# Kernel optimization log

Hardware: AMD Instinct MI355X
Metric: run time of the kernel (lower is better)

Reference implementation:

```python
import jax, jax.numpy as jnp
import numpy as np

EPS = 1e-12  # F.normalize default eps


def build_graph(src, tgt):
    # src,tgt: (b, wh, c). torch does this under no_grad -> stop_gradient.
    logits = jnp.einsum('bnc,bmc->bnm', src, tgt)      # (b, wh, wh)
    g = jax.nn.softmax(logits, axis=-1)                # row softmax
    g = g / jnp.clip(jnp.sum(jnp.abs(g), axis=-2, keepdims=True), EPS)  # L1 norm over dim=-2
    return jax.lax.stop_gradient(g)


def gconv(A, source, message, Wa, ba, Wu, bu):
    # Gconv (PCA-GM style): A @ relu(Linear_a(message)) + relu(Linear_u(source))
    ax = jax.nn.relu(jnp.einsum('bnc,cd->bnd', message, Wa) + ba)
    ux = jax.nn.relu(jnp.einsum('bnc,cd->bnd', source, Wu) + bu)
    return jnp.einsum('bnm,bmd->bnd', A, ax) + ux


def setup_inputs() -> dict:
    key = jax.random.key(0)
    ks = jax.random.split(key, 10)
    b, c, h, w = 4, 256, 64, 64
    scale = 1.0 / np.sqrt(c)
    inp = {
        'skt': jax.random.normal(ks[0], (b, c, h, w), jnp.float32),
        'ref': jax.random.normal(ks[1], (b, c, h, w), jnp.float32),
        'Wa3': jax.random.normal(ks[2], (c, c), jnp.float32) * scale,
        'ba3': jnp.zeros((c,), jnp.float32),
        'Wu3': jax.random.normal(ks[3], (c, c), jnp.float32) * scale,
        'bu3': jnp.zeros((c,), jnp.float32),
        'Wa4': jax.random.normal(ks[4], (c, c), jnp.float32) * scale,
        'ba4': jnp.zeros((c,), jnp.float32),
        'Wu4': jax.random.normal(ks[5], (c, c), jnp.float32) * scale,
        'bu4': jnp.zeros((c,), jnp.float32),
    }
    return inp


def reference(skt, ref, Wa3, ba3, Wu3, bu3, Wa4, ba4, Wu4, bu4):
    b, c, h, w = skt.shape
    skt_f = skt.reshape(b, c, h * w).transpose(0, 2, 1)  # (b, wh, c)
    ref_f = ref.reshape(b, c, h * w).transpose(0, 2, 1)
    sr = build_graph(skt_f, ref_f)                       # (b, wh, wh)
    gen = gconv(sr, skt_f, ref_f, Wa3, ba3, Wu3, bu3) + skt_f
    gg = build_graph(gen, gen)
    ggen = gconv(gg, gen, gen, Wa4, ba4, Wu4, bu4) + gen
    return ggen
```

## Files before the change

kernel.cpp:

```cpp
#include <hip/hip_runtime.h>
#include <cstdint>
#include <cstddef>

#define WH 4096
#define CD 256
typedef long long i64;

typedef __attribute__((ext_vector_type(8))) _Float16 f16x8;
typedef __attribute__((ext_vector_type(4))) float f32x4;

#define AS1 __attribute__((address_space(1)))
#define AS3 __attribute__((address_space(3)))

__device__ __forceinline__ unsigned short f2h(float f) {
    _Float16 h = (_Float16)f;
    return __builtin_bit_cast(unsigned short, h);
}
__device__ __forceinline__ float h2f(unsigned short u) {
    return (float)__builtin_bit_cast(_Float16, u);
}
__device__ __forceinline__ void ld16_lds(const void* g, void* l) {
    __builtin_amdgcn_global_load_lds((AS1 void*)g, (AS3 void*)l, 16, 0, 0);
}

struct TransArgs {
    const float* src[8];
    unsigned short* dhi[8];
    unsigned short* dlo[8];
};
__global__ __launch_bounds__(256) void k_transN(TransArgs ta, int RR, int CC) {
    __shared__ float t[32][33];
    const float* s = ta.src[blockIdx.z];
    unsigned short* dhi = ta.dhi[blockIdx.z];
    unsigned short* dlo = ta.dlo[blockIdx.z];
    const int c0 = blockIdx.x * 32, r0 = blockIdx.y * 32;
    const int tx = threadIdx.x, ty = threadIdx.y;
#pragma unroll
    for (int i = 0; i < 4; ++i)
        t[ty + i * 8][tx] = s[(i64)(r0 + ty + i * 8) * CC + c0 + tx];
    __syncthreads();
#pragma unroll
    for (int i = 0; i < 4; ++i) {
        const i64 idx = (i64)(c0 + ty + i * 8) * RR + r0 + tx;
        const float v = t[tx][ty + i * 8];
        const unsigned short hi = f2h(v);
        dhi[idx] = hi;
        dlo[idx] = f2h(v - h2f(hi));
    }
}

template <int MODE, int SPLIT3>
__global__ __launch_bounds__(256) void k_gemm(
    const unsigned short* __restrict__ A, const unsigned short* __restrict__ A2, int lda, i64 sA,
    const unsigned short* __restrict__ B, const unsigned short* __restrict__ B2, int ldb, i64 sB,
    float* __restrict__ Cf, unsigned short* __restrict__ Chi, unsigned short* __restrict__ Clo,
    int ldc, i64 sC, int K,
    const float* __restrict__ bias,
    const unsigned short* __restrict__ addh, const unsigned short* __restrict__ addl) {
    __shared__ __align__(16) short lA[SPLIT3 ? 8192 : 4096];
    __shared__ __align__(16) short lB[SPLIT3 ? 8192 : 4096];
    const int z = blockIdx.z;
    A += (i64)z * sA; B += (i64)z * sB;
    if constexpr (SPLIT3) { A2 += (i64)z * sA; B2 += (i64)z * sB; }

    const int tid = threadIdx.x;
    const int w = tid >> 6, l = tid & 63;
    const int wm = w >> 1, wn = w & 1;
    const int bm = blockIdx.y * 128, bn = blockIdx.x * 128;
    const int l15 = l & 15, lq = l >> 4;

    f32x4 acc[4][4] = {};

    for (int kt = 0; kt < K; kt += 32) {
        __syncthreads();
#pragma unroll
        for (int rr = 0; rr < 2; ++rr) {
            const int r = w + rr * 4;
            const int kb = r >> 1, mh = r & 1;
            const int row = mh * 64 + l;
            const i64 ao = (i64)(bm + row) * lda + kt + kb * 8;
            const i64 bo = (i64)(bn + row) * ldb + kt + kb * 8;
            ld16_lds(A + ao, (char*)lA + r * 1024);
            ld16_lds(B + bo, (char*)lB + r * 1024);
            if constexpr (SPLIT3) {
                ld16_lds(A2 + ao, (char*)lA + 8192 + r * 1024);
                ld16_lds(B2 + bo, (char*)lB + 8192 + r * 1024);
            }
        }
        __syncthreads();
        f16x8 ah[4], bh[4], al[4], bl[4];
#pragma unroll
        for (int i = 0; i < 4; ++i) {
            const int ia = (lq * 128 + wm * 64 + i * 16 + l15) * 8;
            const int ib = (lq * 128 + wn * 64 + i * 16 + l15) * 8;
            ah[i] = *(const f16x8*)(lA + ia);
            bh[i] = *(const f16x8*)(lB + ib);
            if constexpr (SPLIT3) {
                al[i] = *(const f16x8*)(lA + 4096 + ia);
                bl[i] = *(const f16x8*)(lB + 4096 + ib);
            }
        }
#pragma unroll
        for (int i = 0; i < 4; ++i)
#pragma unroll
            for (int j = 0; j < 4; ++j) {
                acc[i][j] = __builtin_amdgcn_mfma_f32_16x16x32_f16(ah[i], bh[j], acc[i][j], 0, 0, 0);
                if constexpr (SPLIT3) {
                    acc[i][j] = __builtin_amdgcn_mfma_f32_16x16x32_f16(ah[i], bl[j], acc[i][j], 0, 0, 0);
                    acc[i][j] = __builtin_amdgcn_mfma_f32_16x16x32_f16(al[i], bh[j], acc[i][j], 0, 0, 0);
                }
            }
    }

#pragma unroll
    for (int i = 0; i < 4; ++i)
#pragma unroll
        for (int j = 0; j < 4; ++j) {
            const int n = bn + wn * 64 + j * 16 + l15;
            const int m0 = bm + wm * 64 + i * 16 + lq * 4;
            const float bv = bias[n];
            if constexpr (MODE == 1) {
                unsigned short hv[4], lv[4];
#pragma unroll
                for (int r = 0; r < 4; ++r) {
                    const float v = fmaxf(acc[i][j][r] + bv, 0.f);
                    hv[r] = f2h(v);
                    lv[r] = f2h(v - h2f(hv[r]));
                }
                const i64 tb = (i64)z * sC + (i64)n * ldc + m0;
                *(ushort4*)(Chi + tb) = make_ushort4(hv[0], hv[1], hv[2], hv[3]);
                *(ushort4*)(Clo + tb) = make_ushort4(lv[0], lv[1], lv[2], lv[3]);
            } else {
#pragma unroll
                for (int r = 0; r < 4; ++r) {
                    const i64 idx = (i64)z * sC + (i64)(m0 + r) * ldc + n;
                    float v = fmaxf(acc[i][j][r] + bv, 0.f);
                    v += h2f(addh[idx]) + h2f(addl[idx]);
                    Cf[idx] = v;
                }
            }
        }
}

__global__ __launch_bounds__(256) void k_logits(
    const unsigned short* __restrict__ A, const unsigned short* __restrict__ A2,
    const unsigned short* __restrict__ B, const unsigned short* __restrict__ B2,
    unsigned short* __restrict__ G, float2* __restrict__ rowP) {
    __shared__ __align__(16) short lA[8192];
    __shared__ __align__(16) short lB[8192];
    const int tid = threadIdx.x;
    const int w = tid >> 6, l = tid & 63;
    const int wm = w >> 1, wn = w & 1;
    const int bm = blockIdx.y * 128, bn = blockIdx.x * 128;
    const int l15 = l & 15, lq = l >> 4;

    f32x4 acc[4][4] = {};

    for (int kt = 0; kt < CD; kt += 32) {
        __syncthreads();
#pragma unroll
        for (int rr = 0; rr < 2; ++rr) {
            const int r = w + rr * 4;
            const int kb = r >> 1, mh = r & 1;
            const int row = mh * 64 + l;
            const i64 ao = (i64)(bm + row) * CD + kt + kb * 8;
            const i64 bo = (i64)(bn + row) * CD + kt + kb * 8;
            ld16_lds(A + ao, (char*)lA + r * 1024);
            ld16_lds(B + bo, (char*)lB + r * 1024);
            ld16_lds(A2 + ao, (char*)lA + 8192 + r * 1024);
            ld16_lds(B2 + bo, (char*)lB + 8192 + r * 1024);
        }
        __syncthreads();
        f16x8 ah[4], bh[4], al[4], bl[4];
#pragma unroll
        for (int i = 0; i < 4; ++i) {
            const int ia = (lq * 128 + wm * 64 + i * 16 + l15) * 8;
            const int ib = (lq * 128 + wn * 64 + i * 16 + l15) * 8;
            ah[i] = *(const f16x8*)(lA + ia);
            bh[i] = *(const f16x8*)(lB + ib);
            al[i] = *(const f16x8*)(lA + 4096 + ia);
            bl[i] = *(const f16x8*)(lB + 4096 + ib);
        }
#pragma unroll
        for (int i = 0; i < 4; ++i)
#pragma unroll
            for (int j = 0; j < 4; ++j) {
                acc[i][j] = __builtin_amdgcn_mfma_f32_16x16x32_f16(ah[i], bh[j], acc[i][j], 0, 0, 0);
                acc[i][j] = __builtin_amdgcn_mfma_f32_16x16x32_f16(ah[i], bl[j], acc[i][j], 0, 0, 0);
                acc[i][j] = __builtin_amdgcn_mfma_f32_16x16x32_f16(al[i], bh[j], acc[i][j], 0, 0, 0);
            }
    }

#pragma unroll
    for (int i = 0; i < 4; ++i)
#pragma unroll
        for (int r = 0; r < 4; ++r) {
            const int grow = bm + wm * 64 + i * 16 + lq * 4 + r;
            float m = fmaxf(fmaxf(acc[i][0][r], acc[i][1][r]), fmaxf(acc[i][2][r], acc[i][3][r]));
            m = fmaxf(m, __shfl_xor(m, 1));
            m = fmaxf(m, __shfl_xor(m, 2));
            m = fmaxf(m, __shfl_xor(m, 4));
            m = fmaxf(m, __shfl_xor(m, 8));
            float s = 0.f;
#pragma unroll
            for (int j = 0; j < 4; ++j) {
                const float es = __expf((acc[i][j][r] - m) * 0.5f);
                s += es * es;
                G[(i64)grow * WH + bn + wn * 64 + j * 16 + l15] = f2h(es * 256.f);
            }
            s += __shfl_xor(s, 1); s += __shfl_xor(s, 2);
            s += __shfl_xor(s, 4); s += __shfl_xor(s, 8);
            if (l15 == 0)
                rowP[(i64)(blockIdx.x * 2 + wn) * WH + grow] = make_float2(m, s);
        }
}

__global__ __launch_bounds__(256) void k_colpart(const unsigned short* __restrict__ G,
                                                 const float2* __restrict__ rowP,
                                                 float* __restrict__ o,
                                                 float* __restrict__ part) {
    __shared__ float os[64];
    __shared__ float fl[4][64];
    const int t = threadIdx.x;
    const int r0 = blockIdx.y * 64;
    if (t < 64) {
        float M = -3.4e38f, S = 0.f;
        for (int x = 0; x < 64; ++x) {
            const float2 p = rowP[(i64)x * WH + r0 + t];
            const float nm = fmaxf(M, p.x);
            S = S * __expf(M - nm) + p.y * __expf(p.x - nm);
            M = nm;
        }
        const float ov = M + __logf(S);
        os[t] = ov;
        if (blockIdx.x == 0) o[r0 + t] = ov;
    }
    __syncthreads();
    {
        const int jt = t & 3, r = t >> 2;
        fl[jt][r] = __expf(rowP[(i64)(blockIdx.x * 4 + jt) * WH + r0 + r].x - os[r])
                  * (1.f / 65536.f);
    }
    __syncthreads();
    const int j = blockIdx.x * 256 + t;
    const int jt = t >> 6;
    float ps = 0.f;
#pragma unroll 4
    for (int r = 0; r < 64; ++r) {
        const float gv = h2f(G[(i64)(r0 + r) * WH + j]);
        ps += gv * gv * fl[jt][r];
    }
    part[(i64)blockIdx.y * WH + j] = ps;
}

template <int FULL>
__global__ __launch_bounds__(256) void k_attn(
    const unsigned short* __restrict__ G, const float* __restrict__ o,
    const float2* __restrict__ rowP, const float* __restrict__ part,
    const unsigned short* __restrict__ Bh, const unsigned short* __restrict__ Bl,
    float* __restrict__ Pw) {
    __shared__ __align__(16) short lL[4096];
    __shared__ __align__(16) short lBh[4096];
    __shared__ __align__(16) short lBl[FULL ? 4096 : 8];
    __shared__ float lS[512];
    const int tid = threadIdx.x;
    const int w = tid >> 6, l = tid & 63;
    const int wm = w >> 1, wn = w & 1;
    const int bm = blockIdx.y * 128, bn = blockIdx.x * 128;
    const int l15 = l & 15, lq = l >> 4;
    const i64 koff = (i64)blockIdx.z * 512;

    {
        float C0 = 0.f, C1 = 0.f;
#pragma unroll 4
        for (int p = 0; p < 64; ++p) {
            C0 += part[(i64)p * WH + koff + tid];
            C1 += part[(i64)p * WH + koff + 256 + tid];
        }
        lS[tid] = 1.f / fmaxf(C0, 1e-12f);
        lS[tid + 256] = 1.f / fmaxf(C1, 1e-12f);
    }
    float o4[4];
#pragma unroll
    for (int i = 0; i < 4; ++i) o4[i] = o[bm + wm * 64 + i * 16 + l15];

    float fi[4];
    f32x4 acc[4][4] = {};
    for (int kt = 0; kt < 512; kt += 32) {
        __syncthreads();
#pragma unroll
        for (int rr = 0; rr < 2; ++rr) {
            const int r = w + rr * 4;
            const int kb = r >> 1, mh = r & 1;
            ld16_lds(G + (i64)(bm + mh * 64 + l) * WH + koff + kt + kb * 8,
                     (char*)lL + r * 1024);
        }
#pragma unroll
        for (int rr = 0; rr < 2; ++rr) {
            const int r = w + rr * 4;
            const int kb = r >> 1, mh = r & 1;
            const i64 bo = (i64)(bn + mh * 64 + l) * WH + koff + kt + kb * 8;
            ld16_lds(Bh + bo, (char*)lBh + r * 1024);
            if constexpr (FULL) ld16_lds(Bl + bo, (char*)lBl + r * 1024);
        }
        if ((kt & 32) == 0) {
            const i64 half = (koff + kt) >> 6;
#pragma unroll
            for (int i = 0; i < 4; ++i)
                fi[i] = __expf(rowP[half * WH + bm + wm * 64 + i * 16 + l15].x - o4[i])
                      * (1.f / 65536.f);
        }
        __syncthreads();
        float sv[8];
        *(float4*)(sv)     = *(const float4*)(lS + kt + lq * 8);
        *(float4*)(sv + 4) = *(const float4*)(lS + kt + lq * 8 + 4);
        f16x8 bh[4], bl[4];
#pragma unroll
        for (int j = 0; j < 4; ++j) {
            const int ib = (lq * 128 + wn * 64 + j * 16 + l15) * 8;
            bh[j] = *(const f16x8*)(lBh + ib);
            if constexpr (FULL) bl[j] = *(const f16x8*)(lBl + ib);
        }
#pragma unroll
        for (int i = 0; i < 4; ++i) {
            const f16x8 graw = *(const f16x8*)(lL + (lq * 128 + wm * 64 + i * 16 + l15) * 8);
            const float fi_ = fi[i];
            f16x8 ah, al;
#pragma unroll
            for (int e = 0; e < 8; ++e) {
                const float gv = (float)graw[e];
                const float a = gv * gv * fi_ * sv[e];
                const _Float16 hh = (_Float16)a;
                ah[e] = hh;
                if constexpr (FULL) al[e] = (_Float16)(a - (float)hh);
            }
#pragma unroll
            for (int j = 0; j < 4; ++j) {
                acc[i][j] = __builtin_amdgcn_mfma_f32_16x16x32_f16(ah, bh[j], acc[i][j], 0, 0, 0);
                if constexpr (FULL) {
                    acc[i][j] = __builtin_amdgcn_mfma_f32_16x16x32_f16(ah, bl[j], acc[i][j], 0, 0, 0);
                    acc[i][j] = __builtin_amdgcn_mfma_f32_16x16x32_f16(al, bh[j], acc[i][j], 0, 0, 0);
                }
            }
        }
    }
    float* P = Pw + (i64)blockIdx.z * ((i64)WH * CD);
#pragma unroll
    for (int i = 0; i < 4; ++i)
#pragma unroll
        for (int j = 0; j < 4; ++j) {
            const int n = bn + wn * 64 + j * 16 + l15;
            const int m0 = bm + wm * 64 + i * 16 + lq * 4;
#pragma unroll
            for (int r = 0; r < 4; ++r)
                P[(i64)(m0 + r) * CD + n] = acc[i][j][r];
        }
}

template <int SPLIT>
__global__ __launch_bounds__(256) void k_red(const float* __restrict__ Pw,
                                             float* __restrict__ outp,
                                             unsigned short* __restrict__ hi,
                                             unsigned short* __restrict__ lo) {
    const i64 i = ((i64)blockIdx.x * 256 + threadIdx.x) * 4;
    float4 a = *(const float4*)(outp + i);
#pragma unroll
    for (int z = 0; z < 8; ++z) {
        const float4 p = *(const float4*)(Pw + (i64)z * ((i64)WH * CD) + i);
        a.x += p.x; a.y += p.y; a.z += p.z; a.w += p.w;
    }
    *(float4*)(outp + i) = a;
    if constexpr (SPLIT) {
        ushort4 h, l2;
        h.x = f2h(a.x); l2.x = f2h(a.x - h2f(h.x));
        h.y = f2h(a.y); l2.y = f2h(a.y - h2f(h.y));
        h.z = f2h(a.z); l2.z = f2h(a.z - h2f(h.z));
        h.w = f2h(a.w); l2.w = f2h(a.w - h2f(h.w));
        *(ushort4*)(hi + i) = h;
        *(ushort4*)(lo + i) = l2;
    }
}

extern "C" void kernel_launch(void* const* d_in, const int* in_sizes, int n_in,
                              void* d_out, int out_size, void* d_ws, size_t ws_size,
                              hipStream_t stream) {
    (void)in_sizes; (void)n_in; (void)out_size; (void)ws_size;
    const float* skt = (const float*)d_in[0];
    const float* ref = (const float*)d_in[1];
    const float* Wa3 = (const float*)d_in[2];
    const float* ba3 = (const float*)d_in[3];
    const float* Wu3 = (const float*)d_in[4];
    const float* bu3 = (const float*)d_in[5];
    const float* Wa4 = (const float*)d_in[6];
    const float* ba4 = (const float*)d_in[7];
    const float* Wu4 = (const float*)d_in[8];
    const float* bu4 = (const float*)d_in[9];
    float* out = (float*)d_out;

    const i64 WHC = (i64)WH * CD;
    const i64 GM  = (i64)WH * WH;
    const i64 CC  = (i64)CD * CD;

    auto al = [](size_t x) { return (x + 255) & ~(size_t)255; };
    char* p = (char*)d_ws; size_t off = 0;
    auto carve = [&](size_t bytes) { void* r = p + off; off += al(bytes); return r; };
    unsigned short* Gb    = (unsigned short*)carve((size_t)GM * 2);
    unsigned short* skthi = (unsigned short*)carve((size_t)4 * WHC * 2);
    unsigned short* sktlo = (unsigned short*)carve((size_t)4 * WHC * 2);
    unsigned short* refhi = (unsigned short*)carve((size_t)4 * WHC * 2);
    unsigned short* reflo = (unsigned short*)carve((size_t)4 * WHC * 2);
    unsigned short* ghi   = (unsigned short*)carve((size_t)4 * WHC * 2);
    unsigned short* glo   = (unsigned short*)carve((size_t)4 * WHC * 2);
    unsigned short* axthi = (unsigned short*)carve((size_t)4 * WHC * 2);
    unsigned short* axtlo = (unsigned short*)carve((size_t)4 * WHC * 2);
    float* ob             = (float*)carve((size_t)WH * 4);
    float* partb          = (float*)carve((size_t)64 * WH * 4);
    float2* rowPb         = (float2*)carve((size_t)64 * WH * 8);
    unsigned short* Wthi  = (unsigned short*)carve((size_t)4 * CC * 2);
    unsigned short* Wtlo  = (unsigned short*)carve((size_t)4 * CC * 2);
    float* Pw             = (float*)carve((size_t)8 * WHC * 4);

    dim3 thr(256), ttr(32, 8);
    {
        TransArgs ta{};
        for (int b = 0; b < 4; ++b) {
            ta.src[b] = skt + (i64)b * WHC;     ta.src[b + 4] = ref + (i64)b * WHC;
            ta.dhi[b] = skthi + (i64)b * WHC;   ta.dhi[b + 4] = refhi + (i64)b * WHC;
            ta.dlo[b] = sktlo + (i64)b * WHC;   ta.dlo[b + 4] = reflo + (i64)b * WHC;
        }
        k_transN<<<dim3(WH / 32, CD / 32, 8), ttr, 0, stream>>>(ta, CD, WH);
        TransArgs tw{};
        const float* ws[4] = { Wa3, Wu3, Wa4, Wu4 };
        for (int i = 0; i < 4; ++i) {
            tw.src[i] = ws[i];
            tw.dhi[i] = Wthi + (i64)i * CC;
            tw.dlo[i] = Wtlo + (i64)i * CC;
        }
        k_transN<<<dim3(CD / 32, CD / 32, 4), ttr, 0, stream>>>(tw, CD, CD);
    }

    auto stage = [&](const unsigned short* shi, const unsigned short* slo,
                     const unsigned short* mhi, const unsigned short* mlo,
                     int widx, const float* ba, const float* bu, float* outf,
                     unsigned short* ohi, unsigned short* olo, int FULL3) {
        if (FULL3)
            k_gemm<1, 1><<<dim3(CD / 128, WH / 128, 4), thr, 0, stream>>>(
                mhi, mlo, CD, WHC, Wthi + (i64)widx * CC, Wtlo + (i64)widx * CC, CD, 0,
                nullptr, axthi, axtlo, WH, WHC, CD, ba, nullptr, nullptr);
        else
            k_gemm<1, 0><<<dim3(CD / 128, WH / 128, 4), thr, 0, stream>>>(
                mhi, nullptr, CD, WHC, Wthi + (i64)widx * CC, nullptr, CD, 0,
                nullptr, axthi, axtlo, WH, WHC, CD, ba, nullptr, nullptr);
        if (FULL3)
            k_gemm<2, 1><<<dim3(CD / 128, WH / 128, 4), thr, 0, stream>>>(
                shi, slo, CD, WHC, Wthi + (i64)(widx + 1) * CC, Wtlo + (i64)(widx + 1) * CC, CD, 0,
                outf, nullptr, nullptr, CD, WHC, CD, bu, shi, slo);
        else
            k_gemm<2, 0><<<dim3(CD / 128, WH / 128, 4), thr, 0, stream>>>(
                shi, nullptr, CD, WHC, Wthi + (i64)(widx + 1) * CC, nullptr, CD, 0,
                outf, nullptr, nullptr, CD, WHC, CD, bu, shi, slo);
        for (int b = 0; b < 4; ++b) {
            k_logits<<<dim3(WH / 128, WH / 128, 1), thr, 0, stream>>>(
                shi + (i64)b * WHC, slo + (i64)b * WHC,
                mhi + (i64)b * WHC, mlo + (i64)b * WHC, Gb, rowPb);
            k_colpart<<<dim3(WH / 256, WH / 64, 1), thr, 0, stream>>>(Gb, rowPb, ob, partb);
            if (FULL3)
                k_attn<1><<<dim3(CD / 128, WH / 128, 8), thr, 0, stream>>>(
                    Gb, ob, rowPb, partb, axthi + (i64)b * WHC, axtlo + (i64)b * WHC, Pw);
            else
                k_attn<0><<<dim3(CD / 128, WH / 128, 8), thr, 0, stream>>>(
                    Gb, ob, rowPb, partb, axthi + (i64)b * WHC, nullptr, Pw);
            if (ohi)
                k_red<1><<<dim3((unsigned)(WHC / 1024)), thr, 0, stream>>>(
                    Pw, outf + (i64)b * WHC, ohi + (i64)b * WHC, olo + (i64)b * WHC);
            else
                k_red<0><<<dim3((unsigned)(WHC / 1024)), thr, 0, stream>>>(
                    Pw, outf + (i64)b * WHC, nullptr, nullptr);
        }
    };

    stage(skthi, sktlo, refhi, reflo, 0, ba3, bu3, out, ghi, glo, 1);
    stage(ghi, glo, ghi, glo, 2, ba4, bu4, out, nullptr, nullptr, 0);
}
```

Baseline: 1.118 ms.

## Enlarge logits tile to 256 rows and store attention partials in fp16

The logits kernel now computes a 256x128 tile per block with 8x4 accumulators per wave. This reuses each B fragment across twice as many A rows and halves the grid, at the cost of more registers and LDS. Separately, the split-K attention partials are written as fp16 instead of fp32, and the reduction converts them back. That halves partial-buffer traffic but drops precision in the partial sums, which may hurt accuracy.

```diff
diff --git a/kernel.cpp b/kernel.cpp
--- a/kernel.cpp
+++ b/kernel.cpp
@@ -142,60 +142,66 @@
         }
 }
 
-__global__ __launch_bounds__(256) void k_logits(
+__global__ __launch_bounds__(256, 2) void k_logits(
     const unsigned short* __restrict__ A, const unsigned short* __restrict__ A2,
     const unsigned short* __restrict__ B, const unsigned short* __restrict__ B2,
     unsigned short* __restrict__ G, float2* __restrict__ rowP) {
-    __shared__ __align__(16) short lA[8192];
+    __shared__ __align__(16) short lA[16384];
     __shared__ __align__(16) short lB[8192];
     const int tid = threadIdx.x;
     const int w = tid >> 6, l = tid & 63;
     const int wm = w >> 1, wn = w & 1;
-    const int bm = blockIdx.y * 128, bn = blockIdx.x * 128;
+    const int bm = blockIdx.y * 256, bn = blockIdx.x * 128;
     const int l15 = l & 15, lq = l >> 4;
 
-    f32x4 acc[4][4] = {};
+    f32x4 acc[8][4] = {};
 
     for (int kt = 0; kt < CD; kt += 32) {
         __syncthreads();
 #pragma unroll
-        for (int rr = 0; rr < 2; ++rr) {
+        for (int rr = 0; rr < 12; ++rr) {
             const int r = w + rr * 4;
-            const int kb = r >> 1, mh = r & 1;
-            const int row = mh * 64 + l;
-            const i64 ao = (i64)(bm + row) * CD + kt + kb * 8;
-            const i64 bo = (i64)(bn + row) * CD + kt + kb * 8;
-            ld16_lds(A + ao, (char*)lA + r * 1024);
-            ld16_lds(B + bo, (char*)lB + r * 1024);
-            ld16_lds(A2 + ao, (char*)lA + 8192 + r * 1024);
-            ld16_lds(B2 + bo, (char*)lB + 8192 + r * 1024);
-        }
-        __syncthreads();
-        f16x8 ah[4], bh[4], al[4], bl[4];
-#pragma unroll
-        for (int i = 0; i < 4; ++i) {
-            const int ia = (lq * 128 + wm * 64 + i * 16 + l15) * 8;
-            const int ib = (lq * 128 + wn * 64 + i * 16 + l15) * 8;
-            ah[i] = *(const f16x8*)(lA + ia);
-            bh[i] = *(const f16x8*)(lB + ib);
-            al[i] = *(const f16x8*)(lA + 4096 + ia);
-            bl[i] = *(const f16x8*)(lB + 4096 + ib);
-        }
-#pragma unroll
-        for (int i = 0; i < 4; ++i)
+            if (r < 32) {
+                const int ra = r & 15;
+                const int kb = ra >> 2, nh = ra & 3;
+                const i64 ao = (i64)(bm + nh * 64 + l) * CD + kt + kb * 8;
+                if (r < 16) ld16_lds(A + ao, (char*)lA + ra * 1024);
+                else        ld16_lds(A2 + ao, (char*)lA + 16384 + ra * 1024);
+            } else {
+                const int rb = r & 7;
+                const int kb = rb >> 1, mh = rb & 1;
+                const i64 bo = (i64)(bn + mh * 64 + l) * CD + kt + kb * 8;
+                if (r < 40) ld16_lds(B + bo, (char*)lB + rb * 1024);
+                else        ld16_lds(B2 + bo, (char*)lB + 8192 + rb * 1024);
+            }
+        }
+        __syncthreads();
+        f16x8 bh[4], bl[4];
+#pragma unroll
+        for (int j = 0; j < 4; ++j) {
+            const int ib = (lq * 128 + wn * 64 + j * 16 + l15) * 8;
+            bh[j] = *(const f16x8*)(lB + ib);
+            bl[j] = *(const f16x8*)(lB + 4096 + ib);
+        }
+#pragma unroll
+        for (int i = 0; i < 8; ++i) {
+            const int ia = (lq * 256 + wm * 128 + i * 16 + l15) * 8;
+            const f16x8 ah = *(const f16x8*)(lA + ia);
+            const f16x8 al = *(const f16x8*)(lA + 8192 + ia);
 #pragma unroll
             for (int j = 0; j < 4; ++j) {
-                acc[i][j] = __builtin_amdgcn_mfma_f32_16x16x32_f16(ah[i], bh[j], acc[i][j], 0, 0, 0);
-                acc[i][j] = __builtin_amdgcn_mfma_f32_16x16x32_f16(ah[i], bl[j], acc[i][j], 0, 0, 0);
-                acc[i][j] = __builtin_amdgcn_mfma_f32_16x16x32_f16(al[i], bh[j], acc[i][j], 0, 0, 0);
-            }
-    }
-
-#pragma unroll
-    for (int i = 0; i < 4; ++i)
+                acc[i][j] = __builtin_amdgcn_mfma_f32_16x16x32_f16(ah, bh[j], acc[i][j], 0, 0, 0);
+                acc[i][j] = __builtin_amdgcn_mfma_f32_16x16x32_f16(ah, bl[j], acc[i][j], 0, 0, 0);
+                acc[i][j] = __builtin_amdgcn_mfma_f32_16x16x32_f16(al, bh[j], acc[i][j], 0, 0, 0);
+            }
+        }
+    }
+
+#pragma unroll
+    for (int i = 0; i < 8; ++i)
 #pragma unroll
         for (int r = 0; r < 4; ++r) {
-            const int grow = bm + wm * 64 + i * 16 + lq * 4 + r;
+            const int grow = bm + wm * 128 + i * 16 + lq * 4 + r;
             float m = fmaxf(fmaxf(acc[i][0][r], acc[i][1][r]), fmaxf(acc[i][2][r], acc[i][3][r]));
             m = fmaxf(m, __shfl_xor(m, 1));
             m = fmaxf(m, __shfl_xor(m, 2));
@@ -258,7 +264,7 @@
     const unsigned short* __restrict__ G, const float* __restrict__ o,
     const float2* __restrict__ rowP, const float* __restrict__ part,
     const unsigned short* __restrict__ Bh, const unsigned short* __restrict__ Bl,
-    float* __restrict__ Pw) {
+    unsigned short* __restrict__ Pw) {
     __shared__ __align__(16) short lL[4096];
     __shared__ __align__(16) short lBh[4096];
     __shared__ __align__(16) short lBl[FULL ? 4096 : 8];
@@ -344,7 +350,7 @@
             }
         }
     }
-    float* P = Pw + (i64)blockIdx.z * ((i64)WH * CD);
+    unsigned short* P = Pw + (i64)blockIdx.z * ((i64)WH * CD);
 #pragma unroll
     for (int i = 0; i < 4; ++i)
 #pragma unroll
@@ -353,12 +359,12 @@
             const int m0 = bm + wm * 64 + i * 16 + lq * 4;
 #pragma unroll
             for (int r = 0; r < 4; ++r)
-                P[(i64)(m0 + r) * CD + n] = acc[i][j][r];
+                P[(i64)(m0 + r) * CD + n] = f2h(acc[i][j][r]);
         }
 }
 
 template <int SPLIT>
-__global__ __launch_bounds__(256) void k_red(const float* __restrict__ Pw,
+__global__ __launch_bounds__(256) void k_red(const unsigned short* __restrict__ Pw,
                                              float* __restrict__ outp,
                                              unsigned short* __restrict__ hi,
                                              unsigned short* __restrict__ lo) {
@@ -366,8 +372,8 @@
     float4 a = *(const float4*)(outp + i);
 #pragma unroll
     for (int z = 0; z < 8; ++z) {
-        const float4 p = *(const float4*)(Pw + (i64)z * ((i64)WH * CD) + i);
-        a.x += p.x; a.y += p.y; a.z += p.z; a.w += p.w;
+        const ushort4 p = *(const ushort4*)(Pw + (i64)z * ((i64)WH * CD) + i);
+        a.x += h2f(p.x); a.y += h2f(p.y); a.z += h2f(p.z); a.w += h2f(p.w);
     }
     *(float4*)(outp + i) = a;
     if constexpr (SPLIT) {
@@ -418,7 +424,7 @@
     float2* rowPb         = (float2*)carve((size_t)64 * WH * 8);
     unsigned short* Wthi  = (unsigned short*)carve((size_t)4 * CC * 2);
     unsigned short* Wtlo  = (unsigned short*)carve((size_t)4 * CC * 2);
-    float* Pw             = (float*)carve((size_t)8 * WHC * 4);
+    unsigned short* Pw    = (unsigned short*)carve((size_t)8 * WHC * 2);
 
     dim3 thr(256), ttr(32, 8);
     {
@@ -460,7 +466,7 @@
                 shi, nullptr, CD, WHC, Wthi + (i64)(widx + 1) * CC, nullptr, CD, 0,
                 outf, nullptr, nullptr, CD, WHC, CD, bu, shi, slo);
         for (int b = 0; b < 4; ++b) {
-            k_logits<<<dim3(WH / 128, WH / 128, 1), thr, 0, stream>>>(
+            k_logits<<<dim3(WH / 128, WH / 256, 1), thr, 0, stream>>>(
                 shi + (i64)b * WHC, slo + (i64)b * WHC,
                 mhi + (i64)b * WHC, mlo + (i64)b * WHC, Gb, rowPb);
             k_colpart<<<dim3(WH / 256, WH / 64, 1), thr, 0, stream>>>(Gb, rowPb, ob, partb);
```

New measurement: 1.055 ms. 5.6% less time.
